# Performance work log

Hardware: AMD Instinct MI355X
Metric: run time of the kernel (lower is better)

## Reference

```python
import jax, jax.numpy as jnp
import numpy as np

LATENT = 32
GRID = 32
G1 = GRID + 1  # 33 samples per axis (align_corners grid)
HID = 128
N_POINTS = 1048576


def _trilinear_sample(emb, points):
    """Faithful F.grid_sample(mode='bilinear', padding_mode='zeros', align_corners=True).
    emb: [(G1)^3, C] flat table; points: [n,3] in [-1,1], (x,y,z) -> (W,H,D)."""
    C = emb.shape[1]
    # torch .view(1, C, D, H, W) on the flat [(G1)^3 * C] buffer: same reshape here.
    vol = emb.reshape(C, G1, G1, G1).transpose(1, 2, 3, 0)  # [D, H, W, C]
    # align_corners=True: u in [-1,1] -> pixel coord (u+1)/2 * (size-1)
    coords = (points + 1.0) * (0.5 * (G1 - 1))
    x, y, z = coords[:, 0], coords[:, 1], coords[:, 2]
    x0 = jnp.floor(x); y0 = jnp.floor(y); z0 = jnp.floor(z)
    fx = x - x0; fy = y - y0; fz = z - z0
    x0i = x0.astype(jnp.int32); y0i = y0.astype(jnp.int32); z0i = z0.astype(jnp.int32)
    x1i = x0i + 1; y1i = y0i + 1; z1i = z0i + 1

    def corner(zi, yi, xi, w):
        valid = ((zi >= 0) & (zi < G1) & (yi >= 0) & (yi < G1)
                 & (xi >= 0) & (xi < G1))
        zc = jnp.clip(zi, 0, G1 - 1)
        yc = jnp.clip(yi, 0, G1 - 1)
        xc = jnp.clip(xi, 0, G1 - 1)
        v = vol[zc, yc, xc]  # [n, C] gather
        return v * (w * valid.astype(w.dtype))[:, None]

    wx0, wx1 = 1.0 - fx, fx
    wy0, wy1 = 1.0 - fy, fy
    wz0, wz1 = 1.0 - fz, fz
    lat = (corner(z0i, y0i, x0i, wz0 * wy0 * wx0)
           + corner(z0i, y0i, x1i, wz0 * wy0 * wx1)
           + corner(z0i, y1i, x0i, wz0 * wy1 * wx0)
           + corner(z0i, y1i, x1i, wz0 * wy1 * wx1)
           + corner(z1i, y0i, x0i, wz1 * wy0 * wx0)
           + corner(z1i, y0i, x1i, wz1 * wy0 * wx1)
           + corner(z1i, y1i, x0i, wz1 * wy1 * wx0)
           + corner(z1i, y1i, x1i, wz1 * wy1 * wx1))
    return lat  # [n, C]


def setup_inputs() -> dict:
    key = jax.random.key(0)
    ks = jax.random.split(key, 8)
    points = jax.random.uniform(ks[0], (N_POINTS, 3), dtype=jnp.float32)  # in [0,1) subset of [-1,1]
    emb = jax.random.normal(ks[1], (G1 ** 3, LATENT), dtype=jnp.float32)
    w1 = jax.random.normal(ks[2], (LATENT, HID), dtype=jnp.float32) * 0.05
    b1 = jax.random.normal(ks[3], (HID,), dtype=jnp.float32) * 0.05
    w2 = jax.random.normal(ks[4], (HID, HID), dtype=jnp.float32) * 0.05
    b2 = jax.random.normal(ks[5], (HID,), dtype=jnp.float32) * 0.05
    w3 = jax.random.normal(ks[6], (HID, 1), dtype=jnp.float32) * 0.05
    b3 = jax.random.normal(ks[7], (1,), dtype=jnp.float32) * 0.05
    return {"points": points, "emb": emb, "w1": w1, "b1": b1,
            "w2": w2, "b2": b2, "w3": w3, "b3": b3}


def reference(points, emb, w1, b1, w2, b2, w3, b3):
    lat = _trilinear_sample(emb, points)                # [n, latent]
    h = jax.nn.relu(lat @ w1 + b1)                      # [n, hid]
    h = jax.nn.relu(h @ w2 + b2)                        # [n, hid]
    sdf = jnp.tanh(h @ w3 + b3)                         # [n, 1]
    return sdf
```

## Files before the change

kernel.cpp:

```cpp
#include <hip/hip_runtime.h>
#include <hip/hip_bf16.h>

#define NPTS 1048576
#define G1I  33
#define NV   35937
#define NC   32
#define HIDD 128

typedef _Float16 h8  __attribute__((ext_vector_type(8)));
typedef _Float16 h4  __attribute__((ext_vector_type(4)));
typedef __fp16   p2  __attribute__((ext_vector_type(2)));
typedef float    f4  __attribute__((ext_vector_type(4)));

#define WS_A1  0
#define WS_A2  8192
#define WS_EMB 65536
#define WS_NEED (WS_EMB + NV*NC*2)


__global__ __launch_bounds__(256) void vox_prep(
    const float* __restrict__ emb, const float* __restrict__ w1,
    const float* __restrict__ w2, char* __restrict__ ws)
{
    __shared__ _Float16 tile[256][NC];
    const int b = blockIdx.x, t = threadIdx.x;
    _Float16* embh = (_Float16*)(ws + WS_EMB);
    if (b < 141) {
        const int v = b*256 + t;
        #pragma unroll
        for (int c = 0; c < NC; ++c) {
            float val = (v < NV) ? emb[c*NV + v] : 0.f;
            tile[t][c] = (_Float16)val;
        }
        __syncthreads();
        if (v < NV) {
            uint4* dst = (uint4*)(embh + v*NC);
            const uint4* src = (const uint4*)&tile[t][0];
            #pragma unroll
            for (int j = 0; j < 4; ++j) dst[j] = src[j];
        }
    } else if (b < 149) {
        const int t2 = b - 141;
        const int ks = t >> 6, l = t & 63;
        const int gq = l >> 4, colh = l & 15;
        _Float16* a2f = (_Float16*)(ws + WS_A2);
        h8 fr;
        #pragma unroll
        for (int i = 0; i < 8; ++i) {
            const int k = 32*ks + 16*(i>>2) + 4*gq + (i&3);
            fr[i] = (_Float16)w2[k*HIDD + 16*t2 + colh];
        }
        *(h8*)(a2f + ((t2*4+ks)*64 + l)*8) = fr;
    } else {
        _Float16* a1f = (_Float16*)(ws + WS_A1);
        #pragma unroll
        for (int it = 0; it < 2; ++it) {
            const int item = t + it*256;
            const int t8 = item >> 6, l = item & 63;
            const int gq = l >> 4, colh = l & 15;
            h8 fr;
            #pragma unroll
            for (int i = 0; i < 8; ++i) {
                const int k = 16*(i>>2) + 4*gq + (i&3);
                fr[i] = (_Float16)w1[k*HIDD + 16*t8 + colh];
            }
            *(h8*)(a1f + (t8*64 + l)*8) = fr;
        }
    }
}

__global__ __launch_bounds__(256, 2) void vox_main(
    const float* __restrict__ points, const char* __restrict__ ws,
    const float* __restrict__ b1, const float* __restrict__ b2,
    const float* __restrict__ w3, const float* __restrict__ b3v,
    float* __restrict__ out)
{
    __shared__ _Float16 latl[256][40];

    const int tid  = threadIdx.x;
    const int lane = tid & 63;
    const int wv   = tid >> 6;
    const int gq   = lane >> 4;
    const int colh = lane & 15;

    const _Float16* embh = (const _Float16*)(ws + WS_EMB);
    const int p = blockIdx.x*256 + tid;
    const float px = points[3*p+0], py = points[3*p+1], pz = points[3*p+2];
    const float xc = (px + 1.f)*16.f, yc = (py + 1.f)*16.f, zc = (pz + 1.f)*16.f;
    const float xf = floorf(xc), yf = floorf(yc), zf = floorf(zc);
    const float fx = xc - xf, fy = yc - yf, fz = zc - zf;
    const int x0 = (int)xf, y0 = (int)yf, z0 = (int)zf;
    const float wzv[2] = {1.f-fz, fz}, wyv[2] = {1.f-fy, fy}, wxv[2] = {1.f-fx, fx};

    h8 acc8[4];
    #pragma unroll
    for (int j = 0; j < 4; ++j) acc8[j] = (h8){0,0,0,0,0,0,0,0};
    #pragma unroll
    for (int cz = 0; cz < 2; ++cz)
    #pragma unroll
    for (int cy = 0; cy < 2; ++cy) {
        const int vb = ((z0+cz)*G1I + (y0+cy))*G1I + x0;
        const float wzy = wzv[cz]*wyv[cy];
        #pragma unroll
        for (int cx = 0; cx < 2; ++cx) {
            const _Float16 wh = (_Float16)(wzy * wxv[cx]);
            const h8 wp = {wh,wh,wh,wh,wh,wh,wh,wh};
            const h8* rowp = (const h8*)(embh + (vb + cx)*NC);
            #pragma unroll
            for (int j = 0; j < 4; ++j) acc8[j] += wp * rowp[j];
        }
    }
    {
        uint4* lr = (uint4*)&latl[tid][0];
        #pragma unroll
        for (int j = 0; j < 4; ++j) lr[j] = *(uint4*)&acc8[j];
    }
    __syncthreads();

    const h8* a1g = (const h8*)(ws + WS_A1);
    h8 a1fr[8];
    #pragma unroll
    for (int t8 = 0; t8 < 8; ++t8) a1fr[t8] = a1g[t8*64 + lane];
    f4 b1v[8];
    #pragma unroll
    for (int t8 = 0; t8 < 8; ++t8) b1v[t8] = *(const f4*)(b1 + 16*t8 + 4*gq);

    h8 B2f[4][4];
    #pragma unroll
    for (int pt = 0; pt < 4; ++pt) {
        const int row = wv*64 + pt*16 + colh;
        const h4 blo = *(const h4*)&latl[row][4*gq];
        const h4 bhi = *(const h4*)&latl[row][16 + 4*gq];
        h8 bf;
        #pragma unroll
        for (int j = 0; j < 4; ++j) { bf[j] = blo[j]; bf[4+j] = bhi[j]; }
        f4 acc1[8];
        #pragma unroll
        for (int t8 = 0; t8 < 8; ++t8) acc1[t8] = b1v[t8];
        #pragma unroll
        for (int t8 = 0; t8 < 8; ++t8)
            acc1[t8] = __builtin_amdgcn_mfma_f32_16x16x32_f16(a1fr[t8], bf, acc1[t8], 0, 0, 0);
        #pragma unroll
        for (int ks = 0; ks < 4; ++ks) {
            union { h8 v; p2 h[4]; } u;
            const p2 z = {(__fp16)0, (__fp16)0};
            u.h[0] = __builtin_elementwise_max(__builtin_amdgcn_cvt_pkrtz(acc1[2*ks  ][0], acc1[2*ks  ][1]), z);
            u.h[1] = __builtin_elementwise_max(__builtin_amdgcn_cvt_pkrtz(acc1[2*ks  ][2], acc1[2*ks  ][3]), z);
            u.h[2] = __builtin_elementwise_max(__builtin_amdgcn_cvt_pkrtz(acc1[2*ks+1][0], acc1[2*ks+1][1]), z);
            u.h[3] = __builtin_elementwise_max(__builtin_amdgcn_cvt_pkrtz(acc1[2*ks+1][2], acc1[2*ks+1][3]), z);
            B2f[pt][ks] = u.v;
        }
    }

    const h8* a2g = (const h8*)(ws + WS_A2);
    float part[4] = {0.f, 0.f, 0.f, 0.f};
    #pragma unroll
    for (int t2 = 0; t2 < 8; ++t2) {
        const f4 b2q = *(const f4*)(b2 + 16*t2 + 4*gq);
        const f4 w3q = *(const f4*)(w3 + 16*t2 + 4*gq);
        f4 acc2[4];
        #pragma unroll
        for (int pt = 0; pt < 4; ++pt) acc2[pt] = b2q;
        #pragma unroll
        for (int ks = 0; ks < 4; ++ks) {
            const h8 a2fr = a2g[(t2*4 + ks)*64 + lane];
            #pragma unroll
            for (int pt = 0; pt < 4; ++pt)
                acc2[pt] = __builtin_amdgcn_mfma_f32_16x16x32_f16(a2fr, B2f[pt][ks], acc2[pt], 0, 0, 0);
        }
        #pragma unroll
        for (int pt = 0; pt < 4; ++pt)
            #pragma unroll
            for (int r = 0; r < 4; ++r)
                part[pt] += fmaxf(acc2[pt][r], 0.f) * w3q[r];
    }

    float sv = 0.f;
    #pragma unroll
    for (int pt = 0; pt < 4; ++pt) {
        float s = part[pt];
        s += __shfl_xor(s, 16);
        s += __shfl_xor(s, 32);
        if (gq == pt) sv = s;
    }
    const float zi = sv + b3v[0];
    const float e  = __expf(2.f*zi);
    out[blockIdx.x*256 + tid] = (e - 1.f) / (e + 1.f);
}

extern "C" void kernel_launch(void* const* d_in, const int* in_sizes, int n_in,
                              void* d_out, int out_size, void* d_ws, size_t ws_size,
                              hipStream_t stream)
{
    const float* points = (const float*)d_in[0];
    const float* emb    = (const float*)d_in[1];
    const float* w1     = (const float*)d_in[2];
    const float* b1     = (const float*)d_in[3];
    const float* w2     = (const float*)d_in[4];
    const float* b2     = (const float*)d_in[5];
    const float* w3     = (const float*)d_in[6];
    const float* b3     = (const float*)d_in[7];
    float* out = (float*)d_out;
    char*  ws  = (char*)d_ws;
    if (ws_size < (size_t)WS_NEED) return;

    hipLaunchKernelGGL(vox_prep, dim3(150), dim3(256), 0, stream, emb, w1, w2, ws);
    hipLaunchKernelGGL(vox_main, dim3(NPTS/256), dim3(256), 0, stream,
                       points, ws, b1, b2, w3, b3, out);
}
```

Before: 161.5 us.

## Stage W2 fragments in shared LDS, batch corner gathers, and raise occupancy

Each block now loads the layer-2 weight fragments cooperatively, once, into LDS that reuses the latent staging buffer through a union. Previously every wave read the full set from global memory. The eight corner gathers are issued as two batches of four loads per z-slice to expose more memory-level parallelism. Launch bounds go from 2 to 4 blocks per CU, and the b1 bias is reloaded inside the loop to save registers. The first block barrier becomes a wave-local LDS wait, which is safe because each wave only reads the latent rows it wrote. The tighter register budget risks spilling, since the B2 fragments and accumulators are large.

```diff
diff --git a/kernel.cpp b/kernel.cpp
--- a/kernel.cpp
+++ b/kernel.cpp
@@ -69,13 +69,18 @@
     }
 }
 
-__global__ __launch_bounds__(256, 2) void vox_main(
+union SmemU {
+    _Float16 latl[256][40];
+    uint4    a2l[2048];
+};
+
+__global__ __launch_bounds__(256, 4) void vox_main(
     const float* __restrict__ points, const char* __restrict__ ws,
     const float* __restrict__ b1, const float* __restrict__ b2,
     const float* __restrict__ w3, const float* __restrict__ b3v,
     float* __restrict__ out)
 {
-    __shared__ _Float16 latl[256][40];
+    __shared__ SmemU sm;
 
     const int tid  = threadIdx.x;
     const int lane = tid & 63;
@@ -96,47 +101,56 @@
     #pragma unroll
     for (int j = 0; j < 4; ++j) acc8[j] = (h8){0,0,0,0,0,0,0,0};
     #pragma unroll
-    for (int cz = 0; cz < 2; ++cz)
-    #pragma unroll
-    for (int cy = 0; cy < 2; ++cy) {
-        const int vb = ((z0+cz)*G1I + (y0+cy))*G1I + x0;
-        const float wzy = wzv[cz]*wyv[cy];
+    for (int cz = 0; cz < 2; ++cz) {
+        h8 rv[4][4];
+        #pragma unroll
+        for (int cy = 0; cy < 2; ++cy)
         #pragma unroll
         for (int cx = 0; cx < 2; ++cx) {
-            const _Float16 wh = (_Float16)(wzy * wxv[cx]);
+            const h8* rowp = (const h8*)(embh + ((((z0+cz)*G1I) + (y0+cy))*G1I + x0 + cx)*NC);
+            #pragma unroll
+            for (int j = 0; j < 4; ++j) rv[cy*2+cx][j] = rowp[j];
+        }
+        #pragma unroll
+        for (int cy = 0; cy < 2; ++cy)
+        #pragma unroll
+        for (int cx = 0; cx < 2; ++cx) {
+            const _Float16 wh = (_Float16)(wzv[cz]*wyv[cy]*wxv[cx]);
             const h8 wp = {wh,wh,wh,wh,wh,wh,wh,wh};
-            const h8* rowp = (const h8*)(embh + (vb + cx)*NC);
-            #pragma unroll
-            for (int j = 0; j < 4; ++j) acc8[j] += wp * rowp[j];
-        }
-    }
+            #pragma unroll
+            for (int j = 0; j < 4; ++j) acc8[j] += wp * rv[cy*2+cx][j];
+        }
+    }
+
+    const uint4* a2g = (const uint4*)(ws + WS_A2);
+    uint4 a2r[8];
+    #pragma unroll
+    for (int j = 0; j < 8; ++j) a2r[j] = a2g[j*256 + tid];
+
     {
-        uint4* lr = (uint4*)&latl[tid][0];
+        uint4* lr = (uint4*)&sm.latl[tid][0];
         #pragma unroll
         for (int j = 0; j < 4; ++j) lr[j] = *(uint4*)&acc8[j];
     }
-    __syncthreads();
+    asm volatile("s_waitcnt lgkmcnt(0)" ::: "memory");
 
     const h8* a1g = (const h8*)(ws + WS_A1);
     h8 a1fr[8];
     #pragma unroll
     for (int t8 = 0; t8 < 8; ++t8) a1fr[t8] = a1g[t8*64 + lane];
-    f4 b1v[8];
-    #pragma unroll
-    for (int t8 = 0; t8 < 8; ++t8) b1v[t8] = *(const f4*)(b1 + 16*t8 + 4*gq);
 
     h8 B2f[4][4];
     #pragma unroll
     for (int pt = 0; pt < 4; ++pt) {
         const int row = wv*64 + pt*16 + colh;
-        const h4 blo = *(const h4*)&latl[row][4*gq];
-        const h4 bhi = *(const h4*)&latl[row][16 + 4*gq];
+        const h4 blo = *(const h4*)&sm.latl[row][4*gq];
+        const h4 bhi = *(const h4*)&sm.latl[row][16 + 4*gq];
         h8 bf;
         #pragma unroll
         for (int j = 0; j < 4; ++j) { bf[j] = blo[j]; bf[4+j] = bhi[j]; }
         f4 acc1[8];
         #pragma unroll
-        for (int t8 = 0; t8 < 8; ++t8) acc1[t8] = b1v[t8];
+        for (int t8 = 0; t8 < 8; ++t8) acc1[t8] = *(const f4*)(b1 + 16*t8 + 4*gq);
         #pragma unroll
         for (int t8 = 0; t8 < 8; ++t8)
             acc1[t8] = __builtin_amdgcn_mfma_f32_16x16x32_f16(a1fr[t8], bf, acc1[t8], 0, 0, 0);
@@ -152,7 +166,11 @@
         }
     }
 
-    const h8* a2g = (const h8*)(ws + WS_A2);
+    __syncthreads();
+    #pragma unroll
+    for (int j = 0; j < 8; ++j) sm.a2l[j*256 + tid] = a2r[j];
+    __syncthreads();
+
     float part[4] = {0.f, 0.f, 0.f, 0.f};
     #pragma unroll
     for (int t2 = 0; t2 < 8; ++t2) {
@@ -163,7 +181,7 @@
         for (int pt = 0; pt < 4; ++pt) acc2[pt] = b2q;
         #pragma unroll
         for (int ks = 0; ks < 4; ++ks) {
-            const h8 a2fr = a2g[(t2*4 + ks)*64 + lane];
+            const h8 a2fr = *(const h8*)&sm.a2l[(t2*4 + ks)*64 + lane];
             #pragma unroll
             for (int pt = 0; pt < 4; ++pt)
                 acc2[pt] = __builtin_amdgcn_mfma_f32_16x16x32_f16(a2fr, B2f[pt][ks], acc2[pt], 0, 0, 0);
```

Result: slower. 203.0 us (+25.6%).
